# Performance work log

Measured on AMD Instinct MI355X. Metric: run time of the kernel, lower is better.

Reference implementation:

```python
import jax, jax.numpy as jnp
import numpy as np

TAGSET = 64
START_TAG = 62
STOP_TAG = 63
B, S = 32, 256


def setup_inputs() -> dict:
    key = jax.random.key(0)
    k1, k2, k3 = jax.random.split(key, 3)
    features = jax.random.normal(k1, (B, S, TAGSET, TAGSET), dtype=jnp.float32)
    targets = jax.random.randint(k2, (B, S), 0, TAGSET * TAGSET, dtype=jnp.int64)
    lengths = jax.random.randint(k3, (B,), 1, S + 1, dtype=jnp.int64)
    # pack_padded_sequence requires lengths sorted descending; ensure max length = S
    lengths = jnp.sort(lengths)[::-1].at[0].set(S)
    return {"features": features, "targets": targets, "lengths": lengths}


def reference(features, targets, lengths):
    Bc, Sc, T, _ = features.shape
    # --- gold score: gather the score of the true (from_tag, to_tag) pair per token ---
    flat = features.reshape(Bc, Sc, T * T)                       # [B,S,T*T]
    scores_at_targets = jnp.take_along_axis(flat, targets[:, :, None], axis=2)[..., 0]
    valid = (jnp.arange(Sc)[None, :] < lengths[:, None])          # [B,S] pad mask
    gold_score = jnp.sum(jnp.where(valid, scores_at_targets, 0.0))

    # --- CRF forward algorithm (log-sum-exp recurrence over time) ---
    init = features[:, 0, START_TAG, :]                           # [B,T] (all lengths >= 1)
    feats_t = jnp.swapaxes(features, 0, 1)[1:]                    # [S-1,B,T,T]
    active = (jnp.arange(1, Sc)[:, None] < lengths[None, :])       # [S-1,B]

    def step(scores, inp):
        feat, act = inp                                           # feat [B,T,T], act [B]
        new = jax.nn.logsumexp(feat + scores[:, :, None], axis=1)  # lse over from-tag
        scores = jnp.where(act[:, None], new, scores)
        return scores, None

    scores_upto_t, _ = jax.lax.scan(step, init, (feats_t, active))
    all_paths_scores = jnp.sum(scores_upto_t[:, STOP_TAG])

    return (all_paths_scores - gold_score) / Bc
```

## Files before the change

### kernel.cpp

```cpp
#include <hip/hip_runtime.h>
#include <cmath>

#define NB 32
#define NS 256
#define NT 64
#define START_TAG 62
#define STOP_TAG 63
#define CL 8
#define NCH 32
#define GS 8.0f
#define LOG64 4.1588830833596715f

typedef __attribute__((ext_vector_type(8))) short short8;
typedef __attribute__((ext_vector_type(4))) float float4v;

union FragU { unsigned u[4]; short8 s; unsigned short h[8]; };

__device__ inline unsigned pkbf(float a, float b) {
  unsigned ua = (__float_as_uint(a) + 0x8000u) >> 16;
  unsigned ub = (__float_as_uint(b) + 0x8000u) & 0xffff0000u;
  return ua | ub;
}

__global__ __launch_bounds__(256) void chunk_kernel(
    const float* __restrict__ feat, const int* __restrict__ lengths,
    unsigned short* __restrict__ cmat) {
  const int wv  = threadIdx.x >> 6;
  const int gid = blockIdx.x * 4 + wv;
  const int b   = gid >> 5;
  const int c   = gid & 31;
  const int len = lengths[b];
  const int t1  = 1 + c * CL;
  const int nmat = min(len, t1 + CL) - t1;
  if (nmat <= 0) return;

  const int lane = threadIdx.x & 63;
  const int q  = lane >> 4;
  const int cc = lane & 15;

  const float* fb = feat + ((size_t)b * NS + t1) * (NT * NT);

  FragU BQ[2][4];
  #pragma unroll
  for (int h = 0; h < 2; ++h)
    #pragma unroll
    for (int tj = 0; tj < 4; ++tj) {
      const float* p = fb + (16 * tj + cc) * NT + 32 * h + 8 * q;
      float4 x = *(const float4*)p;
      float4 y = *(const float4*)(p + 4);
      BQ[h][tj].u[0] = pkbf(__expf(x.x - GS), __expf(x.y - GS));
      BQ[h][tj].u[1] = pkbf(__expf(x.z - GS), __expf(x.w - GS));
      BQ[h][tj].u[2] = pkbf(__expf(y.x - GS), __expf(y.y - GS));
      BQ[h][tj].u[3] = pkbf(__expf(y.z - GS), __expf(y.w - GS));
    }

  float raw[4][2][8];
  if (nmat > 1) {
    const float* p = fb + NT * NT;
    #pragma unroll
    for (int mi = 0; mi < 4; ++mi)
      #pragma unroll
      for (int kh = 0; kh < 2; ++kh)
        #pragma unroll
        for (int j = 0; j < 8; ++j)
          raw[mi][kh][j] = p[(32 * kh + 8 * q + j) * NT + 16 * mi + cc];
  }

  const int src0 = (((q & 1) * 2) << 4) | cc;
  const int src1 = src0 + 16;
  const bool hi = (q >> 1) != 0;

  for (int k = 1; k < nmat; ++k) {
    FragU FA[4][2];
    #pragma unroll
    for (int mi = 0; mi < 4; ++mi)
      #pragma unroll
      for (int kh = 0; kh < 2; ++kh)
        #pragma unroll
        for (int j2 = 0; j2 < 4; ++j2)
          FA[mi][kh].u[j2] =
              pkbf(__expf(raw[mi][kh][2 * j2]     - (GS + LOG64)),
                   __expf(raw[mi][kh][2 * j2 + 1] - (GS + LOG64)));

    if (k + 1 < nmat) {
      const float* p = fb + (size_t)(k + 1) * (NT * NT);
      #pragma unroll
      for (int mi = 0; mi < 4; ++mi)
        #pragma unroll
        for (int kh = 0; kh < 2; ++kh)
          #pragma unroll
          for (int j = 0; j < 8; ++j)
            raw[mi][kh][j] = p[(32 * kh + 8 * q + j) * NT + 16 * mi + cc];
    }

    float4v acc[4][4];
    #pragma unroll
    for (int ti = 0; ti < 4; ++ti)
      #pragma unroll
      for (int tj = 0; tj < 4; ++tj) {
        float4v z = {0.f, 0.f, 0.f, 0.f};
        z = __builtin_amdgcn_mfma_f32_16x16x32_bf16(FA[ti][0].s, BQ[0][tj].s, z, 0, 0, 0);
        acc[ti][tj] = __builtin_amdgcn_mfma_f32_16x16x32_bf16(FA[ti][1].s, BQ[1][tj].s, z, 0, 0, 0);
      }

    unsigned pk01[4][4], pk23[4][4];
    #pragma unroll
    for (int ti = 0; ti < 4; ++ti)
      #pragma unroll
      for (int tj = 0; tj < 4; ++tj) {
        pk01[ti][tj] = pkbf(acc[ti][tj][0], acc[ti][tj][1]);
        pk23[ti][tj] = pkbf(acc[ti][tj][2], acc[ti][tj][3]);
      }

    #pragma unroll
    for (int h = 0; h < 2; ++h)
      #pragma unroll
      for (int tj = 0; tj < 4; ++tj) {
        unsigned a0 = (unsigned)__shfl((int)pk01[2 * h][tj],     src0);
        unsigned b0 = (unsigned)__shfl((int)pk01[2 * h + 1][tj], src0);
        unsigned a1 = (unsigned)__shfl((int)pk23[2 * h][tj],     src0);
        unsigned b1 = (unsigned)__shfl((int)pk23[2 * h + 1][tj], src0);
        unsigned a2 = (unsigned)__shfl((int)pk01[2 * h][tj],     src1);
        unsigned b2 = (unsigned)__shfl((int)pk01[2 * h + 1][tj], src1);
        unsigned a3 = (unsigned)__shfl((int)pk23[2 * h][tj],     src1);
        unsigned b3 = (unsigned)__shfl((int)pk23[2 * h + 1][tj], src1);
        BQ[h][tj].u[0] = hi ? b0 : a0;
        BQ[h][tj].u[1] = hi ? b1 : a1;
        BQ[h][tj].u[2] = hi ? b2 : a2;
        BQ[h][tj].u[3] = hi ? b3 : a3;
      }
  }

  unsigned short* dst = cmat + ((size_t)b * NCH + c) * (NT * NT);
  #pragma unroll
  for (int h = 0; h < 2; ++h)
    #pragma unroll
    for (int tj = 0; tj < 4; ++tj)
      #pragma unroll
      for (int j = 0; j < 8; ++j)
        dst[(32 * h + 8 * q + j) * NT + 16 * tj + cc] = BQ[h][tj].h[j];
}

__global__ __launch_bounds__(64) void combine_kernel(
    const float* __restrict__ feat, const int* __restrict__ targets,
    const int* __restrict__ lengths, const unsigned int* __restrict__ cmat,
    float* __restrict__ out) {
  const int b = blockIdx.x;
  const int j = threadIdx.x;
  __shared__ float sv[NT];
  const int len = lengths[b];
  const float* f0 = feat + (size_t)b * NS * (NT * NT);

  float gold = 0.f;
  #pragma unroll
  for (int g = 0; g < 4; ++g) {
    const int s = j + 64 * g;
    if (s < len) {
      const int tgt = targets[b * NS + s];
      gold += f0[(size_t)s * (NT * NT) + tgt];
    }
  }

  float x = f0[START_TAG * NT + j];
  float m = x;
  #pragma unroll
  for (int off = 32; off; off >>= 1) m = fmaxf(m, __shfl_xor(m, off));
  float v = __expf(x - m);
  float L = m;

  const int nch = (len - 1 + CL - 1) / CL;
  uint4 Q0[8];
  if (nch > 0) {
    const uint4* P = (const uint4*)cmat + (size_t)b * NCH * 512 + j * 8;
    #pragma unroll
    for (int w = 0; w < 8; ++w) Q0[w] = P[w];
  }

  for (int c2 = 0; c2 < nch; ++c2) {
    sv[j] = v;
    __builtin_amdgcn_wave_barrier();

    uint4 Q1[8];
    if (c2 + 1 < nch) {
      const uint4* P = (const uint4*)cmat + ((size_t)b * NCH + c2 + 1) * 512 + j * 8;
      #pragma unroll
      for (int w = 0; w < 8; ++w) Q1[w] = P[w];
    }

    float ac0 = 0.f, ac1 = 0.f, ac2 = 0.f, ac3 = 0.f;
    const float4* svp = (const float4*)sv;
    #pragma unroll
    for (int w = 0; w < 8; ++w) {
      uint4 qq = Q0[w];
      float4 s0 = svp[2 * w], s1 = svp[2 * w + 1];
      ac0 = fmaf(__uint_as_float(qq.x << 16), s0.x, ac0);
      ac1 = fmaf(__uint_as_float(qq.x & 0xffff0000u), s0.y, ac1);
      ac2 = fmaf(__uint_as_float(qq.y << 16), s0.z, ac2);
      ac3 = fmaf(__uint_as_float(qq.y & 0xffff0000u), s0.w, ac3);
      ac0 = fmaf(__uint_as_float(qq.z << 16), s1.x, ac0);
      ac1 = fmaf(__uint_as_float(qq.z & 0xffff0000u), s1.y, ac1);
      ac2 = fmaf(__uint_as_float(qq.w << 16), s1.z, ac2);
      ac3 = fmaf(__uint_as_float(qq.w & 0xffff0000u), s1.w, ac3);
    }
    float acc = (ac0 + ac1) + (ac2 + ac3);
    __builtin_amdgcn_wave_barrier();

    const int tt1 = 1 + c2 * CL;
    const int nmat = min(len, tt1 + CL) - tt1;
    L += (float)nmat * GS + (float)(nmat - 1) * LOG64;

    float mm = acc;
    #pragma unroll
    for (int off = 32; off; off >>= 1) mm = fmaxf(mm, __shfl_xor(mm, off));
    v = acc / mm;
    L += __logf(mm);

    #pragma unroll
    for (int w = 0; w < 8; ++w) Q0[w] = Q1[w];
  }

  float lv = __logf(v);
  float path = L + __shfl(lv, STOP_TAG);

  #pragma unroll
  for (int off = 32; off; off >>= 1) gold += __shfl_down(gold, off);
  if (j == 0) atomicAdd(out, (path - gold) * (1.0f / (float)NB));
}

extern "C" void kernel_launch(void* const* d_in, const int* in_sizes, int n_in,
                              void* d_out, int out_size, void* d_ws, size_t ws_size,
                              hipStream_t stream) {
  const float* feat    = (const float*)d_in[0];
  const int*   targets = (const int*)d_in[1];
  const int*   lengths = (const int*)d_in[2];
  unsigned short* cmat = (unsigned short*)d_ws;
  float* out = (float*)d_out;

  hipMemsetAsync(d_out, 0, sizeof(float), stream);
  chunk_kernel<<<NB * NCH / 4, 256, 0, stream>>>(feat, lengths, cmat);
  combine_kernel<<<NB, 64, 0, stream>>>(feat, targets, lengths,
                                        (const unsigned int*)cmat, out);
}
```

Before: 223.4 us.

## Fuse chunk and combine kernels via last-arriving-wave atomic counter

Merges the chunk-matrix kernel and the per-batch combine kernel into one launch. Each wave atomically increments a per-batch counter after writing its chunk matrix, and the last of the 32 waves runs the sequential combine for that batch. The combine loop now keeps three chunk matrices prefetched instead of one. This removes a kernel launch and its tail gap, at the cost of an extra memset, threadfences, and a combine that runs as a single wave inside a 256-thread block.

After: 260.7 us. 1.17x slower.

```diff
diff --git a/kernel.cpp b/kernel.cpp
--- a/kernel.cpp
+++ b/kernel.cpp
@@ -10,6 +10,7 @@
 #define NCH 32
 #define GS 8.0f
 #define LOG64 4.1588830833596715f
+#define CMAT_SHORTS ((size_t)NB * NCH * NT * NT)
 
 typedef __attribute__((ext_vector_type(8))) short short8;
 typedef __attribute__((ext_vector_type(4))) float float4v;
@@ -22,9 +23,10 @@
   return ua | ub;
 }
 
-__global__ __launch_bounds__(256) void chunk_kernel(
-    const float* __restrict__ feat, const int* __restrict__ lengths,
-    unsigned short* __restrict__ cmat) {
+__global__ __launch_bounds__(256) void crf_fused(
+    const float* __restrict__ feat, const int* __restrict__ targets,
+    const int* __restrict__ lengths, unsigned short* __restrict__ cmat,
+    unsigned int* __restrict__ cnt, float* __restrict__ out) {
   const int wv  = threadIdx.x >> 6;
   const int gid = blockIdx.x * 4 + wv;
   const int b   = gid >> 5;
@@ -32,58 +34,33 @@
   const int len = lengths[b];
   const int t1  = 1 + c * CL;
   const int nmat = min(len, t1 + CL) - t1;
-  if (nmat <= 0) return;
 
   const int lane = threadIdx.x & 63;
   const int q  = lane >> 4;
   const int cc = lane & 15;
 
-  const float* fb = feat + ((size_t)b * NS + t1) * (NT * NT);
-
-  FragU BQ[2][4];
-  #pragma unroll
-  for (int h = 0; h < 2; ++h)
-    #pragma unroll
-    for (int tj = 0; tj < 4; ++tj) {
-      const float* p = fb + (16 * tj + cc) * NT + 32 * h + 8 * q;
-      float4 x = *(const float4*)p;
-      float4 y = *(const float4*)(p + 4);
-      BQ[h][tj].u[0] = pkbf(__expf(x.x - GS), __expf(x.y - GS));
-      BQ[h][tj].u[1] = pkbf(__expf(x.z - GS), __expf(x.w - GS));
-      BQ[h][tj].u[2] = pkbf(__expf(y.x - GS), __expf(y.y - GS));
-      BQ[h][tj].u[3] = pkbf(__expf(y.z - GS), __expf(y.w - GS));
-    }
-
-  float raw[4][2][8];
-  if (nmat > 1) {
-    const float* p = fb + NT * NT;
-    #pragma unroll
-    for (int mi = 0; mi < 4; ++mi)
-      #pragma unroll
-      for (int kh = 0; kh < 2; ++kh)
-        #pragma unroll
-        for (int j = 0; j < 8; ++j)
-          raw[mi][kh][j] = p[(32 * kh + 8 * q + j) * NT + 16 * mi + cc];
-  }
-
-  const int src0 = (((q & 1) * 2) << 4) | cc;
-  const int src1 = src0 + 16;
-  const bool hi = (q >> 1) != 0;
-
-  for (int k = 1; k < nmat; ++k) {
-    FragU FA[4][2];
-    #pragma unroll
-    for (int mi = 0; mi < 4; ++mi)
-      #pragma unroll
-      for (int kh = 0; kh < 2; ++kh)
-        #pragma unroll
-        for (int j2 = 0; j2 < 4; ++j2)
-          FA[mi][kh].u[j2] =
-              pkbf(__expf(raw[mi][kh][2 * j2]     - (GS + LOG64)),
-                   __expf(raw[mi][kh][2 * j2 + 1] - (GS + LOG64)));
-
-    if (k + 1 < nmat) {
-      const float* p = fb + (size_t)(k + 1) * (NT * NT);
+  __shared__ float sv[NT];
+
+  if (nmat > 0) {
+    const float* fb = feat + ((size_t)b * NS + t1) * (NT * NT);
+
+    FragU BQ[2][4];
+    #pragma unroll
+    for (int h = 0; h < 2; ++h)
+      #pragma unroll
+      for (int tj = 0; tj < 4; ++tj) {
+        const float* p = fb + (16 * tj + cc) * NT + 32 * h + 8 * q;
+        float4 x = *(const float4*)p;
+        float4 y = *(const float4*)(p + 4);
+        BQ[h][tj].u[0] = pkbf(__expf(x.x - GS), __expf(x.y - GS));
+        BQ[h][tj].u[1] = pkbf(__expf(x.z - GS), __expf(x.w - GS));
+        BQ[h][tj].u[2] = pkbf(__expf(y.x - GS), __expf(y.y - GS));
+        BQ[h][tj].u[3] = pkbf(__expf(y.z - GS), __expf(y.w - GS));
+      }
+
+    float raw[4][2][8];
+    if (nmat > 1) {
+      const float* p = fb + NT * NT;
       #pragma unroll
       for (int mi = 0; mi < 4; ++mi)
         #pragma unroll
@@ -93,62 +70,89 @@
             raw[mi][kh][j] = p[(32 * kh + 8 * q + j) * NT + 16 * mi + cc];
     }
 
-    float4v acc[4][4];
-    #pragma unroll
-    for (int ti = 0; ti < 4; ++ti)
-      #pragma unroll
-      for (int tj = 0; tj < 4; ++tj) {
-        float4v z = {0.f, 0.f, 0.f, 0.f};
-        z = __builtin_amdgcn_mfma_f32_16x16x32_bf16(FA[ti][0].s, BQ[0][tj].s, z, 0, 0, 0);
-        acc[ti][tj] = __builtin_amdgcn_mfma_f32_16x16x32_bf16(FA[ti][1].s, BQ[1][tj].s, z, 0, 0, 0);
+    const int src0 = (((q & 1) * 2) << 4) | cc;
+    const int src1 = src0 + 16;
+    const bool hi = (q >> 1) != 0;
+
+    for (int k = 1; k < nmat; ++k) {
+      FragU FA[4][2];
+      #pragma unroll
+      for (int mi = 0; mi < 4; ++mi)
+        #pragma unroll
+        for (int kh = 0; kh < 2; ++kh)
+          #pragma unroll
+          for (int j2 = 0; j2 < 4; ++j2)
+            FA[mi][kh].u[j2] =
+                pkbf(__expf(raw[mi][kh][2 * j2]     - (GS + LOG64)),
+                     __expf(raw[mi][kh][2 * j2 + 1] - (GS + LOG64)));
+
+      if (k + 1 < nmat) {
+        const float* p = fb + (size_t)(k + 1) * (NT * NT);
+        #pragma unroll
+        for (int mi = 0; mi < 4; ++mi)
+          #pragma unroll
+          for (int kh = 0; kh < 2; ++kh)
+            #pragma unroll
+            for (int j = 0; j < 8; ++j)
+              raw[mi][kh][j] = p[(32 * kh + 8 * q + j) * NT + 16 * mi + cc];
       }
 
-    unsigned pk01[4][4], pk23[4][4];
-    #pragma unroll
-    for (int ti = 0; ti < 4; ++ti)
-      #pragma unroll
-      for (int tj = 0; tj < 4; ++tj) {
-        pk01[ti][tj] = pkbf(acc[ti][tj][0], acc[ti][tj][1]);
-        pk23[ti][tj] = pkbf(acc[ti][tj][2], acc[ti][tj][3]);
-      }
-
+      float4v acc[4][4];
+      #pragma unroll
+      for (int ti = 0; ti < 4; ++ti)
+        #pragma unroll
+        for (int tj = 0; tj < 4; ++tj) {
+          float4v z = {0.f, 0.f, 0.f, 0.f};
+          z = __builtin_amdgcn_mfma_f32_16x16x32_bf16(FA[ti][0].s, BQ[0][tj].s, z, 0, 0, 0);
+          acc[ti][tj] = __builtin_amdgcn_mfma_f32_16x16x32_bf16(FA[ti][1].s, BQ[1][tj].s, z, 0, 0, 0);
+        }
+
+      unsigned pk01[4][4], pk23[4][4];
+      #pragma unroll
+      for (int ti = 0; ti < 4; ++ti)
+        #pragma unroll
+        for (int tj = 0; tj < 4; ++tj) {
+          pk01[ti][tj] = pkbf(acc[ti][tj][0], acc[ti][tj][1]);
+          pk23[ti][tj] = pkbf(acc[ti][tj][2], acc[ti][tj][3]);
+        }
+
+      #pragma unroll
+      for (int h = 0; h < 2; ++h)
+        #pragma unroll
+        for (int tj = 0; tj < 4; ++tj) {
+          unsigned a0 = (unsigned)__shfl((int)pk01[2 * h][tj],     src0);
+          unsigned b0 = (unsigned)__shfl((int)pk01[2 * h + 1][tj], src0);
+          unsigned a1 = (unsigned)__shfl((int)pk23[2 * h][tj],     src0);
+          unsigned b1 = (unsigned)__shfl((int)pk23[2 * h + 1][tj], src0);
+          unsigned a2 = (unsigned)__shfl((int)pk01[2 * h][tj],     src1);
+          unsigned b2 = (unsigned)__shfl((int)pk01[2 * h + 1][tj], src1);
+          unsigned a3 = (unsigned)__shfl((int)pk23[2 * h][tj],     src1);
+          unsigned b3 = (unsigned)__shfl((int)pk23[2 * h + 1][tj], src1);
+          BQ[h][tj].u[0] = hi ? b0 : a0;
+          BQ[h][tj].u[1] = hi ? b1 : a1;
+          BQ[h][tj].u[2] = hi ? b2 : a2;
+          BQ[h][tj].u[3] = hi ? b3 : a3;
+        }
+    }
+
+    unsigned short* dst = cmat + ((size_t)b * NCH + c) * (NT * NT);
     #pragma unroll
     for (int h = 0; h < 2; ++h)
       #pragma unroll
-      for (int tj = 0; tj < 4; ++tj) {
-        unsigned a0 = (unsigned)__shfl((int)pk01[2 * h][tj],     src0);
-        unsigned b0 = (unsigned)__shfl((int)pk01[2 * h + 1][tj], src0);
-        unsigned a1 = (unsigned)__shfl((int)pk23[2 * h][tj],     src0);
-        unsigned b1 = (unsigned)__shfl((int)pk23[2 * h + 1][tj], src0);
-        unsigned a2 = (unsigned)__shfl((int)pk01[2 * h][tj],     src1);
-        unsigned b2 = (unsigned)__shfl((int)pk01[2 * h + 1][tj], src1);
-        unsigned a3 = (unsigned)__shfl((int)pk23[2 * h][tj],     src1);
-        unsigned b3 = (unsigned)__shfl((int)pk23[2 * h + 1][tj], src1);
-        BQ[h][tj].u[0] = hi ? b0 : a0;
-        BQ[h][tj].u[1] = hi ? b1 : a1;
-        BQ[h][tj].u[2] = hi ? b2 : a2;
-        BQ[h][tj].u[3] = hi ? b3 : a3;
-      }
+      for (int tj = 0; tj < 4; ++tj)
+        #pragma unroll
+        for (int j = 0; j < 8; ++j)
+          dst[(32 * h + 8 * q + j) * NT + 16 * tj + cc] = BQ[h][tj].h[j];
   }
 
-  unsigned short* dst = cmat + ((size_t)b * NCH + c) * (NT * NT);
-  #pragma unroll
-  for (int h = 0; h < 2; ++h)
-    #pragma unroll
-    for (int tj = 0; tj < 4; ++tj)
-      #pragma unroll
-      for (int j = 0; j < 8; ++j)
-        dst[(32 * h + 8 * q + j) * NT + 16 * tj + cc] = BQ[h][tj].h[j];
-}
-
-__global__ __launch_bounds__(64) void combine_kernel(
-    const float* __restrict__ feat, const int* __restrict__ targets,
-    const int* __restrict__ lengths, const unsigned int* __restrict__ cmat,
-    float* __restrict__ out) {
-  const int b = blockIdx.x;
-  const int j = threadIdx.x;
-  __shared__ float sv[NT];
-  const int len = lengths[b];
+  __threadfence();
+  unsigned old = 0;
+  if (lane == 0) old = atomicAdd(&cnt[b], 1u);
+  old = (unsigned)__shfl((int)old, 0);
+  if (old != NCH - 1) return;
+  __threadfence();
+
+  const int j = lane;
   const float* f0 = feat + (size_t)b * NS * (NT * NT);
 
   float gold = 0.f;
@@ -169,29 +173,24 @@
   float L = m;
 
   const int nch = (len - 1 + CL - 1) / CL;
-  uint4 Q0[8];
-  if (nch > 0) {
-    const uint4* P = (const uint4*)cmat + (size_t)b * NCH * 512 + j * 8;
-    #pragma unroll
-    for (int w = 0; w < 8; ++w) Q0[w] = P[w];
-  }
-
-  for (int c2 = 0; c2 < nch; ++c2) {
+  const uint4* base = (const uint4*)(cmat + (size_t)b * NCH * (NT * NT)) + j * 8;
+
+  uint4 QA[8], QB[8], QC[8];
+  auto LQ = [&](uint4* D, int c2) {
+    if (c2 < nch) {
+      const uint4* P = base + (size_t)c2 * 512;
+      #pragma unroll
+      for (int w = 0; w < 8; ++w) D[w] = P[w];
+    }
+  };
+  auto STEP = [&](const uint4* Q, int c2) {
     sv[j] = v;
     __builtin_amdgcn_wave_barrier();
-
-    uint4 Q1[8];
-    if (c2 + 1 < nch) {
-      const uint4* P = (const uint4*)cmat + ((size_t)b * NCH + c2 + 1) * 512 + j * 8;
-      #pragma unroll
-      for (int w = 0; w < 8; ++w) Q1[w] = P[w];
-    }
-
     float ac0 = 0.f, ac1 = 0.f, ac2 = 0.f, ac3 = 0.f;
     const float4* svp = (const float4*)sv;
     #pragma unroll
     for (int w = 0; w < 8; ++w) {
-      uint4 qq = Q0[w];
+      uint4 qq = Q[w];
       float4 s0 = svp[2 * w], s1 = svp[2 * w + 1];
       ac0 = fmaf(__uint_as_float(qq.x << 16), s0.x, ac0);
       ac1 = fmaf(__uint_as_float(qq.x & 0xffff0000u), s0.y, ac1);
@@ -204,19 +203,22 @@
     }
     float acc = (ac0 + ac1) + (ac2 + ac3);
     __builtin_amdgcn_wave_barrier();
-
     const int tt1 = 1 + c2 * CL;
-    const int nmat = min(len, tt1 + CL) - tt1;
-    L += (float)nmat * GS + (float)(nmat - 1) * LOG64;
-
+    const int nm = min(len, tt1 + CL) - tt1;
+    L += (float)nm * GS + (float)(nm - 1) * LOG64;
     float mm = acc;
     #pragma unroll
     for (int off = 32; off; off >>= 1) mm = fmaxf(mm, __shfl_xor(mm, off));
     v = acc / mm;
     L += __logf(mm);
-
-    #pragma unroll
-    for (int w = 0; w < 8; ++w) Q0[w] = Q1[w];
+  };
+
+  LQ(QA, 0); LQ(QB, 1); LQ(QC, 2);
+  for (int c2 = 0; c2 < nch; c2 += 3) {
+    STEP(QA, c2);
+    LQ(QA, c2 + 3);
+    if (c2 + 1 < nch) { STEP(QB, c2 + 1); LQ(QB, c2 + 4); }
+    if (c2 + 2 < nch) { STEP(QC, c2 + 2); LQ(QC, c2 + 5); }
   }
 
   float lv = __logf(v);
@@ -234,10 +236,10 @@
   const int*   targets = (const int*)d_in[1];
   const int*   lengths = (const int*)d_in[2];
   unsigned short* cmat = (unsigned short*)d_ws;
+  unsigned int* cnt = (unsigned int*)((char*)d_ws + CMAT_SHORTS * 2);
   float* out = (float*)d_out;
 
+  hipMemsetAsync(cnt, 0, NB * sizeof(unsigned int), stream);
   hipMemsetAsync(d_out, 0, sizeof(float), stream);
-  chunk_kernel<<<NB * NCH / 4, 256, 0, stream>>>(feat, lengths, cmat);
-  combine_kernel<<<NB, 64, 0, stream>>>(feat, targets, lengths,
-                                        (const unsigned int*)cmat, out);
+  crf_fused<<<NB * NCH / 4, 256, 0, stream>>>(feat, targets, lengths, cmat, cnt, out);
 }
```
